# Kernel tuning notes

Measured on AMD Instinct MI355X. Metric: run time of the kernel, lower is better.

The kernel has to match this reference:

```python
import jax, jax.numpy as jnp
import numpy as np

T, B, E, H = 2048, 2, 1024, 16
D = E // H
MAX_REL = 16  # RelativePosition default max_relative_position


def setup_inputs() -> dict:
    key = jax.random.key(0)
    ks = jax.random.split(key, 11)
    s = 1.0 / np.sqrt(E)
    inp = {
        'query': jax.random.normal(ks[0], (T, B, E), dtype=jnp.float32),
        'Wq': jax.random.normal(ks[1], (E, E), dtype=jnp.float32) * s,
        'bq': jnp.zeros((E,), dtype=jnp.float32),
        'Wk': jax.random.normal(ks[2], (E, E), dtype=jnp.float32) * s,
        'bk': jnp.zeros((E,), dtype=jnp.float32),
        'Wv': jax.random.normal(ks[3], (E, E), dtype=jnp.float32) * s,
        'bv': jnp.zeros((E,), dtype=jnp.float32),
        'Wo': jax.random.normal(ks[4], (E, E), dtype=jnp.float32) * s,
        'bo': jnp.zeros((E,), dtype=jnp.float32),
        'rk_table': jax.random.normal(ks[5], (2 * MAX_REL + 1, D), dtype=jnp.float32) * 0.05,
        'rv_table': jax.random.normal(ks[6], (2 * MAX_REL + 1, D), dtype=jnp.float32) * 0.05,
    }
    return inp


def _rel_idx(lq, lk):
    # distance_mat = k - q, clipped to [-MAX_REL, MAX_REL], shifted to [0, 2*MAX_REL]
    d = jnp.arange(lk)[None, :] - jnp.arange(lq)[:, None]
    return jnp.clip(d, -MAX_REL, MAX_REL) + MAX_REL  # [lq, lk] int


def reference(query, Wq, bq, Wk, bk, Wv, bv, Wo, bo, rk_table, rv_table):
    t, b, e = query.shape
    scale = D ** -0.5
    # projections (torch Linear: x @ W.T + b)
    q = (query @ Wq.T + bq) * scale
    k = query @ Wk.T + bk
    v = query @ Wv.T + bv
    # [T,B,E] -> [B*H, T, D]
    q = q.reshape(t, b * H, D).transpose(1, 0, 2)
    k = k.reshape(t, b * H, D).transpose(1, 0, 2)
    v = v.reshape(t, b * H, D).transpose(1, 0, 2)
    # content scores + Shaw relative-position key scores
    scores = jnp.einsum('ntd,nsd->nts', q, k)            # [N, T, S]
    rk = rk_table[_rel_idx(t, t)]                        # [T, S, D]
    scores = scores + jnp.einsum('ntd,tsd->nts', q, rk)  # relpos_k term
    probs = jax.nn.softmax(scores, axis=-1)
    # weighted values + Shaw relative-position value term
    rv = rv_table[_rel_idx(t, t)]                        # [T, S, D]
    attn = jnp.einsum('nts,nsd->ntd', probs, v) + jnp.einsum('nts,tsd->ntd', probs, rv)
    # [B*H, T, D] -> [T, B, E]
    attn = attn.transpose(1, 0, 2).reshape(t, b, e)
    return attn @ Wo.T + bo
```

## Files before the change

kernel.cpp:

```cpp
#include <hip/hip_runtime.h>
#include <hip/hip_bf16.h>
#include <math.h>

#define T_   2048
#define B_   2
#define E_   1024
#define H_   16
#define D_   64
#define NH_  32
#define M_   4096

typedef __attribute__((ext_vector_type(8))) short s8b;
typedef __attribute__((ext_vector_type(4))) float f4;

#define MFMA_B16(a,b,c) __builtin_amdgcn_mfma_f32_16x16x32_bf16(a,b,c,0,0,0)
#define LOG2E 1.44269504088896f

__device__ __forceinline__ unsigned short f2bu(float f) {
    union { __hip_bfloat16 h; unsigned short u; } cv;
    cv.h = __float2bfloat16(f);
    return cv.u;
}
__device__ __forceinline__ float bu2f(unsigned short u) {
    union { __hip_bfloat16 h; unsigned short u; } cv; cv.u = u;
    return __bfloat162float(cv.h);
}
__device__ __forceinline__ unsigned int pk2(float a, float b) {
    return (unsigned int)f2bu(a) | ((unsigned int)f2bu(b) << 16);
}
__device__ __forceinline__ float ld1d(const void* p, size_t idx, bool f32) {
    return f32 ? ((const float*)p)[idx] : bu2f(((const unsigned short*)p)[idx]);
}
__device__ __forceinline__ float qsum16(float v) {
    v += __shfl_xor(v, 1); v += __shfl_xor(v, 2);
    v += __shfl_xor(v, 4); v += __shfl_xor(v, 8);
    return v;
}

__global__ void detect_dtype(const unsigned short* __restrict__ q, int* __restrict__ flag) {
    int e = (q[threadIdx.x] >> 7) & 0xFF;
    bool sane = (e == 0) || (e >= 97 && e <= 157);
    unsigned long long m = __ballot(sane);
    if (threadIdx.x == 0) *flag = (__popcll(m) >= 56) ? 0 : 1;
}

__global__ __launch_bounds__(256) void cvt_bf16(
    const void* __restrict__ x,
    const void* __restrict__ Wq, const void* __restrict__ Wk,
    const void* __restrict__ Wv, const void* __restrict__ Wo,
    const void* __restrict__ bq, const void* __restrict__ bk,
    const void* __restrict__ bv, const void* __restrict__ bo,
    unsigned short* __restrict__ xw, unsigned short* __restrict__ Ww,
    unsigned short* __restrict__ bw, const int* __restrict__ flag)
{
    const bool f32m = (*flag != 0);
    const int y = blockIdx.y;
    const void* src; unsigned short* dst; int n;
    if (y == 0)      { src = x; dst = xw; n = M_ * E_; }
    else if (y <= 4) {
        src = (y == 1) ? Wq : (y == 2) ? Wk : (y == 3) ? Wv : Wo;
        dst = Ww + (size_t)(y - 1) * E_ * E_; n = E_ * E_;
    } else {
        src = (y == 5) ? bq : (y == 6) ? bk : (y == 7) ? bv : bo;
        dst = bw + (size_t)(y - 5) * E_; n = E_;
    }
    int i = (blockIdx.x * 256 + threadIdx.x) * 8;
    if (i >= n) return;
    if (f32m) {
        const float* s = (const float*)src + i;
        float4 f0 = *(const float4*)s, f1 = *(const float4*)(s + 4);
        union { unsigned int d[4]; s8b v; } u;
        u.d[0] = pk2(f0.x, f0.y); u.d[1] = pk2(f0.z, f0.w);
        u.d[2] = pk2(f1.x, f1.y); u.d[3] = pk2(f1.z, f1.w);
        *(s8b*)(dst + i) = u.v;
    } else {
        *(s8b*)(dst + i) = *(const s8b*)((const unsigned short*)src + i);
    }
}

__global__ __launch_bounds__(256, 3) void qkv_gemm(
    const unsigned short* __restrict__ xw, const unsigned short* __restrict__ Ww,
    const unsigned short* __restrict__ bw,
    unsigned short* __restrict__ qo, unsigned short* __restrict__ ko,
    unsigned short* __restrict__ vo)
{
    const int bid = blockIdx.x;
    const int r = bid & 7, s = bid >> 3;
    const int g = r + 8 * (s >> 3);
    const int e0 = (s & 7) * 128;
    const int m0 = (g & 31) * 128;
    const int p  = g >> 5;
    const unsigned short* W    = Ww + (size_t)p * E_ * E_;
    const unsigned short* bias = bw + (size_t)p * E_;
    unsigned short* dst = (p == 0) ? qo : (p == 1) ? ko : vo;
    const float scale = (p == 0) ? 0.125f * LOG2E : 1.0f;

    const int tid = threadIdx.x, w = tid >> 6, lane = tid & 63;
    const int quad = lane >> 4, lc = lane & 15;
    const int wx = w & 1, wy = w >> 1;

    __shared__ unsigned short a_s[2][128 * 36];
    __shared__ unsigned short b_s[2][128 * 36];

    f4 acc[4][4];
    #pragma unroll
    for (int i = 0; i < 4; i++)
        #pragma unroll
        for (int j = 0; j < 4; j++) acc[i][j] = (f4){0.f, 0.f, 0.f, 0.f};

    const int lrow = tid >> 1, lcb = (tid & 1) * 16;
    const size_t abase = (size_t)(m0 + lrow) * E_ + lcb;
    const size_t bbase = (size_t)(e0 + lrow) * E_ + lcb;

    s8b pA0 = *(const s8b*)(xw + abase);
    s8b pA1 = *(const s8b*)(xw + abase + 8);
    s8b pB0 = *(const s8b*)(W + bbase);
    s8b pB1 = *(const s8b*)(W + bbase + 8);
    *(s8b*)&a_s[0][lrow * 36 + lcb]     = pA0;
    *(s8b*)&a_s[0][lrow * 36 + lcb + 8] = pA1;
    *(s8b*)&b_s[0][lrow * 36 + lcb]     = pB0;
    *(s8b*)&b_s[0][lrow * 36 + lcb + 8] = pB1;
    __syncthreads();

    for (int k0 = 0; k0 < E_; k0 += 32) {
        const int cur = (k0 >> 5) & 1;
        if (k0 + 32 < E_) {
            pA0 = *(const s8b*)(xw + abase + k0 + 32);
            pA1 = *(const s8b*)(xw + abase + k0 + 40);
            pB0 = *(const s8b*)(W + bbase + k0 + 32);
            pB1 = *(const s8b*)(W + bbase + k0 + 40);
        }
        s8b af[4], bfr[4];
        #pragma unroll
        for (int i = 0; i < 4; i++) af[i]  = *(const s8b*)&a_s[cur][(wy*64 + i*16 + lc)*36 + quad*8];
        #pragma unroll
        for (int i = 0; i < 4; i++) bfr[i] = *(const s8b*)&b_s[cur][(wx*64 + i*16 + lc)*36 + quad*8];
        #pragma unroll
        for (int ms = 0; ms < 4; ms++)
            #pragma unroll
            for (int ns = 0; ns < 4; ns++)
                acc[ms][ns] = MFMA_B16(af[ms], bfr[ns], acc[ms][ns]);
        if (k0 + 32 < E_) {
            *(s8b*)&a_s[cur ^ 1][lrow * 36 + lcb]     = pA0;
            *(s8b*)&a_s[cur ^ 1][lrow * 36 + lcb + 8] = pA1;
            *(s8b*)&b_s[cur ^ 1][lrow * 36 + lcb]     = pB0;
            *(s8b*)&b_s[cur ^ 1][lrow * 36 + lcb + 8] = pB1;
        }
        __syncthreads();
    }

    float bias_v[4];
    #pragma unroll
    for (int ns = 0; ns < 4; ns++) bias_v[ns] = bu2f(bias[e0 + wx*64 + ns*16 + lc]);

    #pragma unroll
    for (int ms = 0; ms < 4; ms++)
        #pragma unroll
        for (int ns = 0; ns < 4; ns++)
            #pragma unroll
            for (int r2 = 0; r2 < 4; r2++) {
                float val = (acc[ms][ns][r2] + bias_v[ns]) * scale;
                float nb = __shfl_xor(val, 1);
                if (!(lane & 1)) {
                    int m = m0 + wy*64 + ms*16 + quad*4 + r2;
                    int t = m >> 1, bb = m & 1;
                    int e = e0 + wx*64 + ns*16 + lc;
                    int h = e >> 6, d = e & 63;
                    *(unsigned int*)&dst[(((size_t)(bb*H_ + h) * T_ + t) << 6) + d] = pk2(val, nb);
                }
            }
}

__global__ __launch_bounds__(256, 2) void attn_mfma(
    const unsigned short* __restrict__ q, const unsigned short* __restrict__ k,
    const unsigned short* __restrict__ v,
    const void* __restrict__ rk_t, const void* __restrict__ rv_t,
    unsigned short* __restrict__ aout, const int* __restrict__ flag)
{
    const bool f32m = (*flag != 0);
    const int bid = blockIdx.x;
    const int n = bid & 31, qt = bid >> 5;
    const int t0 = qt * 128;
    const int tid = threadIdx.x, w = tid >> 6, lane = tid & 63;
    const int quad = lane >> 4, lc = lane & 15;

    __shared__ unsigned short k_s[2][64 * 72];
    __shared__ unsigned short v_t[2][64 * 72];
    __shared__ unsigned short p_s[4][32 * 72];
    __shared__ unsigned short qrk_s[128 * 36];
    __shared__ unsigned short diag16[128 * 33];
    __shared__ float st_L[128], st_R[128];

    const unsigned short* qn = q + ((size_t)n * T_ + t0) * D_;
    const unsigned short* kn = k + (size_t)n * T_ * D_;
    const unsigned short* vn = v + (size_t)n * T_ * D_;

    s8b qa[2][2];
    #pragma unroll
    for (int mt = 0; mt < 2; mt++)
        #pragma unroll
        for (int kf = 0; kf < 2; kf++)
            qa[mt][kf] = *(const s8b*)(qn + (size_t)(w*32 + mt*16 + lc) * D_ + kf*32 + quad*8);

    for (int i = tid; i < 128 * 33; i += 256) diag16[i] = 0;

    unsigned int* rks = (unsigned int*)&p_s[0][0];
    for (int i = tid; i < 48 * 36; i += 256) {
        int r = i / 36, c2 = i % 36;
        unsigned int val = 0;
        if (r < 33 && c2 < 32)
            val = pk2(ld1d(rk_t, r*64 + 2*c2, f32m), ld1d(rk_t, r*64 + 2*c2 + 1, f32m));
        rks[i] = val;
    }
    __syncthreads();

    #pragma unroll
    for (int mt = 0; mt < 2; mt++)
        for (int nt = 0; nt < 3; nt++) {
            s8b b0 = *(const s8b*)((const unsigned short*)rks + (nt*16 + lc)*72 + quad*8);
            s8b b1 = *(const s8b*)((const unsigned short*)rks + (nt*16 + lc)*72 + 32 + quad*8);
            f4 a = (f4){0.f, 0.f, 0.f, 0.f};
            a = MFMA_B16(qa[mt][0], b0, a);
            a = MFMA_B16(qa[mt][1], b1, a);
            #pragma unroll
            for (int r = 0; r < 4; r++) {
                float nb = __shfl_xor(a[r], 1);
                int col = nt*16 + lc;
                if (!(lane & 1) && col < 34)
                    ((unsigned int*)qrk_s)[(w*32 + mt*16 + quad*4 + r)*18 + (col >> 1)] = pk2(a[r], nb);
            }
        }
    __syncthreads();

    float qL[2][4], qR[2][4];
    float L_p[2][4] = {}, R_p[2][4] = {};
    f4 O[2][4], lsN[2], lsL[2], lsR[2];
    #pragma unroll
    for (int mt = 0; mt < 2; mt++) {
        #pragma unroll
        for (int r = 0; r < 4; r++) {
            int row = w*32 + mt*16 + quad*4 + r;
            qL[mt][r] = bu2f(qrk_s[row*36 + 0]);
            qR[mt][r] = bu2f(qrk_s[row*36 + 32]);
        }
        lsN[mt] = (f4){0.f, 0.f, 0.f, 0.f};
        lsL[mt] = (f4){0.f, 0.f, 0.f, 0.f};
        lsR[mt] = (f4){0.f, 0.f, 0.f, 0.f};
        #pragma unroll
        for (int dt = 0; dt < 4; dt++) O[mt][dt] = (f4){0.f, 0.f, 0.f, 0.f};
    }
    const short ob = (short)0x3F80;
    const s8b ones = { ob, ob, ob, ob, ob, ob, ob, ob };

    const int ks_ = tid >> 2, kdq = (tid & 3) * 16;
    const int vsp = (tid & 31) * 2, vd0 = (tid >> 5) * 8;
    s8b kr0 = *(const s8b*)(kn + ks_*64 + kdq);
    s8b kr1 = *(const s8b*)(kn + ks_*64 + kdq + 8);
    s8b vr0 = *(const s8b*)(vn + vsp*64 + vd0);
    s8b vr1 = *(const s8b*)(vn + (vsp + 1)*64 + vd0);
    *(s8b*)&k_s[0][ks_*72 + kdq]     = kr0;
    *(s8b*)&k_s[0][ks_*72 + kdq + 8] = kr1;
    #pragma unroll
    for (int i = 0; i < 8; i++)
        ((unsigned int*)v_t[0])[(vd0 + i)*36 + (vsp >> 1)] =
            (unsigned int)(unsigned short)vr0[i] | ((unsigned int)(unsigned short)vr1[i] << 16);
    __syncthreads();

    for (int kt = 0; kt < 32; kt++) {
        const int s0 = kt * 64;
        const int cur = kt & 1;
        if (kt + 1 < 32) {
            const unsigned short* kp = kn + (size_t)(s0 + 64) * D_;
            const unsigned short* vp = vn + (size_t)(s0 + 64) * D_;
            kr0 = *(const s8b*)(kp + ks_*64 + kdq);
            kr1 = *(const s8b*)(kp + ks_*64 + kdq + 8);
            vr0 = *(const s8b*)(vp + vsp*64 + vd0);
            vr1 = *(const s8b*)(vp + (vsp + 1)*64 + vd0);
        }

        const bool farL  = (s0 + 63 < t0 - 16);
        const bool farR  = (s0 > t0 + 143);
        const bool nearT = !farL && !farR;

        s8b bk[4][2];
        #pragma unroll
        for (int st = 0; st < 4; st++) {
            bk[st][0] = *(const s8b*)&k_s[cur][(st*16 + lc)*72 + quad*8];
            bk[st][1] = *(const s8b*)&k_s[cur][(st*16 + lc)*72 + 32 + quad*8];
        }

        #pragma unroll
        for (int mt = 0; mt < 2; mt++) {
            if (!nearT) {
                const float* qb = farL ? qL[mt] : qR[mt];
                f4 ini = (f4){qb[0], qb[1], qb[2], qb[3]};
                #pragma unroll
                for (int st = 0; st < 4; st++) {
                    f4 a = MFMA_B16(qa[mt][0], bk[st][0], ini);
                    a = MFMA_B16(qa[mt][1], bk[st][1], a);
                    #pragma unroll
                    for (int r = 0; r < 4; r++)
                        p_s[w][(mt*16 + quad*4 + r)*72 + st*16 + lc] = f2bu(exp2f(a[r]));
                }
            } else {
                #pragma unroll
                for (int st = 0; st < 4; st++) {
                    f4 a = (f4){0.f, 0.f, 0.f, 0.f};
                    a = MFMA_B16(qa[mt][0], bk[st][0], a);
                    a = MFMA_B16(qa[mt][1], bk[st][1], a);
                    #pragma unroll
                    for (int r = 0; r < 4; r++) {
                        int t_l = w*32 + mt*16 + quad*4 + r;
                        int rel = (s0 + st*16 + lc) - (t0 + t_l);
                        int rc = rel < -16 ? -16 : (rel > 16 ? 16 : rel);
                        float e = exp2f(a[r] + bu2f(qrk_s[t_l*36 + rc + 16]));
                        unsigned short eb = f2bu(e);
                        if (rel <= -16)      L_p[mt][r] += e;
                        else if (rel >= 16)  R_p[mt][r] += e;
                        else                 diag16[t_l*33 + rel + 15] = eb;
                        p_s[w][(mt*16 + quad*4 + r)*72 + st*16 + lc] = eb;
                    }
                }
            }
        }

        s8b pa[2][2];
        #pragma unroll
        for (int mt = 0; mt < 2; mt++) {
            pa[mt][0] = *(const s8b*)&p_s[w][(mt*16 + lc)*72 + quad*8];
            pa[mt][1] = *(const s8b*)&p_s[w][(mt*16 + lc)*72 + 32 + quad*8];
        }
        if (nearT) {
            #pragma unroll
            for (int mt = 0; mt < 2; mt++) {
                lsN[mt] = MFMA_B16(pa[mt][0], ones, lsN[mt]);
                lsN[mt] = MFMA_B16(pa[mt][1], ones, lsN[mt]);
            }
        } else if (farL) {
            #pragma unroll
            for (int mt = 0; mt < 2; mt++) {
                lsL[mt] = MFMA_B16(pa[mt][0], ones, lsL[mt]);
                lsL[mt] = MFMA_B16(pa[mt][1], ones, lsL[mt]);
            }
        } else {
            #pragma unroll
            for (int mt = 0; mt < 2; mt++) {
                lsR[mt] = MFMA_B16(pa[mt][0], ones, lsR[mt]);
                lsR[mt] = MFMA_B16(pa[mt][1], ones, lsR[mt]);
            }
        }
        #pragma unroll
        for (int dt = 0; dt < 4; dt++) {
            s8b b0 = *(const s8b*)&v_t[cur][(dt*16 + lc)*72 + quad*8];
            s8b b1 = *(const s8b*)&v_t[cur][(dt*16 + lc)*72 + 32 + quad*8];
            O[0][dt] = MFMA_B16(pa[0][0], b0, O[0][dt]);
            O[0][dt] = MFMA_B16(pa[0][1], b1, O[0][dt]);
            O[1][dt] = MFMA_B16(pa[1][0], b0, O[1][dt]);
            O[1][dt] = MFMA_B16(pa[1][1], b1, O[1][dt]);
        }

        if (kt + 1 < 32) {
            *(s8b*)&k_s[cur ^ 1][ks_*72 + kdq]     = kr0;
            *(s8b*)&k_s[cur ^ 1][ks_*72 + kdq + 8] = kr1;
            #pragma unroll
            for (int i = 0; i < 8; i++)
                ((unsigned int*)v_t[cur ^ 1])[(vd0 + i)*36 + (vsp >> 1)] =
                    (unsigned int)(unsigned short)vr0[i] | ((unsigned int)(unsigned short)vr1[i] << 16);
        }
        __syncthreads();
    }

    float linv[2][4];
    #pragma unroll
    for (int mt = 0; mt < 2; mt++)
        #pragma unroll
        for (int r = 0; r < 4; r++) {
            float l = lsN[mt][r] + lsL[mt][r] + lsR[mt][r];
            float L = lsL[mt][r] + qsum16(L_p[mt][r]);
            float R = lsR[mt][r] + qsum16(R_p[mt][r]);
            linv[mt][r] = 1.f / l;
            if (lc == 0) {
                int row = w*32 + mt*16 + quad*4 + r;
                st_L[row] = L; st_R[row] = R;
            }
        }
    {
        unsigned int* rvs = (unsigned int*)&k_s[0][0];
        for (int i = tid; i < 64 * 36; i += 256) {
            int d = i / 36, c2 = i % 36;
            int r0 = 2 * c2, r1 = 2 * c2 + 1;
            float x0 = (r0 < 33) ? ld1d(rv_t, (size_t)r0 * 64 + d, f32m) : 0.f;
            float x1 = (r1 < 33) ? ld1d(rv_t, (size_t)r1 * 64 + d, f32m) : 0.f;
            rvs[i] = pk2(x0, x1);
        }
    }
    __syncthreads();
    for (int j = 0; j < 32; j++) {
        int c = lane;
        int row = w*32 + j;
        unsigned short pv;
        if (c == 0)        pv = f2bu(st_L[row]);
        else if (c == 32)  pv = f2bu(st_R[row]);
        else if (c < 32)   pv = diag16[row*33 + c - 1];
        else               pv = 0;
        p_s[w][j*72 + c] = pv;
    }
    s8b pa[2][2];
    #pragma unroll
    for (int mt = 0; mt < 2; mt++) {
        pa[mt][0] = *(const s8b*)&p_s[w][(mt*16 + lc)*72 + quad*8];
        pa[mt][1] = *(const s8b*)&p_s[w][(mt*16 + lc)*72 + 32 + quad*8];
    }
    #pragma unroll
    for (int dt = 0; dt < 4; dt++) {
        s8b b0 = *(const s8b*)&k_s[0][(dt*16 + lc)*72 + quad*8];
        s8b b1 = *(const s8b*)&k_s[0][(dt*16 + lc)*72 + 32 + quad*8];
        O[0][dt] = MFMA_B16(pa[0][0], b0, O[0][dt]);
        O[0][dt] = MFMA_B16(pa[0][1], b1, O[0][dt]);
        O[1][dt] = MFMA_B16(pa[1][0], b0, O[1][dt]);
        O[1][dt] = MFMA_B16(pa[1][1], b1, O[1][dt]);
    }
    const int bb = n >> 4, h = n & 15;
    #pragma unroll
    for (int mt = 0; mt < 2; mt++)
        #pragma unroll
        for (int r = 0; r < 4; r++) {
            int t_g = t0 + w*32 + mt*16 + quad*4 + r;
            #pragma unroll
            for (int dt = 0; dt < 4; dt++) {
                float val = O[mt][dt][r] * linv[mt][r];
                float nb = __shfl_xor(val, 1);
                if (!(lane & 1)) {
                    int e = h*64 + dt*16 + lc;
                    *(unsigned int*)&aout[((size_t)t_g * B_ + bb) * E_ + e] = pk2(val, nb);
                }
            }
        }
}

__global__ __launch_bounds__(256, 3) void out_gemm(
    const unsigned short* __restrict__ A,
    const unsigned short* __restrict__ Wob, const unsigned short* __restrict__ bob,
    void* __restrict__ out, const int* __restrict__ flag)
{
    const bool f32m = (*flag != 0);
    const int bid = blockIdx.x;
    const int r = bid & 7, s = bid >> 3;
    const int g = r + 8 * (s >> 3);
    const int m0 = g * 128;
    const int e0 = (s & 7) * 128;

    const int tid = threadIdx.x, w = tid >> 6, lane = tid & 63;
    const int quad = lane >> 4, lc = lane & 15;
    const int wx = w & 1, wy = w >> 1;

    __shared__ unsigned short a_s[2][128 * 36];
    __shared__ unsigned short b_s[2][128 * 36];

    f4 acc[4][4];
    #pragma unroll
    for (int i = 0; i < 4; i++)
        #pragma unroll
        for (int j = 0; j < 4; j++) acc[i][j] = (f4){0.f, 0.f, 0.f, 0.f};

    const int lrow = tid >> 1, lcb = (tid & 1) * 16;
    const size_t abase = (size_t)(m0 + lrow) * E_ + lcb;
    const size_t bbase = (size_t)(e0 + lrow) * E_ + lcb;

    s8b pA0 = *(const s8b*)(A + abase);
    s8b pA1 = *(const s8b*)(A + abase + 8);
    s8b pB0 = *(const s8b*)(Wob + bbase);
    s8b pB1 = *(const s8b*)(Wob + bbase + 8);
    *(s8b*)&a_s[0][lrow*36 + lcb]     = pA0;
    *(s8b*)&a_s[0][lrow*36 + lcb + 8] = pA1;
    *(s8b*)&b_s[0][lrow*36 + lcb]     = pB0;
    *(s8b*)&b_s[0][lrow*36 + lcb + 8] = pB1;
    __syncthreads();

    for (int k0 = 0; k0 < E_; k0 += 32) {
        const int cur = (k0 >> 5) & 1;
        if (k0 + 32 < E_) {
            pA0 = *(const s8b*)(A + abase + k0 + 32);
            pA1 = *(const s8b*)(A + abase + k0 + 40);
            pB0 = *(const s8b*)(Wob + bbase + k0 + 32);
            pB1 = *(const s8b*)(Wob + bbase + k0 + 40);
        }
        s8b af[4], bfr[4];
        #pragma unroll
        for (int i = 0; i < 4; i++) af[i]  = *(const s8b*)&a_s[cur][(wy*64 + i*16 + lc)*36 + quad*8];
        #pragma unroll
        for (int i = 0; i < 4; i++) bfr[i] = *(const s8b*)&b_s[cur][(wx*64 + i*16 + lc)*36 + quad*8];
        #pragma unroll
        for (int ms = 0; ms < 4; ms++)
            #pragma unroll
            for (int ns = 0; ns < 4; ns++)
                acc[ms][ns] = MFMA_B16(af[ms], bfr[ns], acc[ms][ns]);
        if (k0 + 32 < E_) {
            *(s8b*)&a_s[cur ^ 1][lrow*36 + lcb]     = pA0;
            *(s8b*)&a_s[cur ^ 1][lrow*36 + lcb + 8] = pA1;
            *(s8b*)&b_s[cur ^ 1][lrow*36 + lcb]     = pB0;
            *(s8b*)&b_s[cur ^ 1][lrow*36 + lcb + 8] = pB1;
        }
        __syncthreads();
    }

    float bias_v[4];
    #pragma unroll
    for (int ns = 0; ns < 4; ns++) bias_v[ns] = bu2f(bob[e0 + wx*64 + ns*16 + lc]);

    #pragma unroll
    for (int ms = 0; ms < 4; ms++)
        #pragma unroll
        for (int ns = 0; ns < 4; ns++)
            #pragma unroll
            for (int r2 = 0; r2 < 4; r2++) {
                float val = acc[ms][ns][r2] + bias_v[ns];
                size_t m = m0 + wy*64 + ms*16 + quad*4 + r2;
                int e = e0 + wx*64 + ns*16 + lc;
                if (f32m) {
                    ((float*)out)[m * E_ + e] = val;
                } else {
                    float nb = __shfl_xor(val, 1);
                    if (!(lane & 1))
                        *(unsigned int*)&((unsigned short*)out)[m * E_ + e] = pk2(val, nb);
                }
            }
}

extern "C" void kernel_launch(void* const* d_in, const int* in_sizes, int n_in,
                              void* d_out, int out_size, void* d_ws, size_t ws_size,
                              hipStream_t stream) {
    const void* x  = d_in[0];
    const void* Wq = d_in[1];  const void* bq = d_in[2];
    const void* Wk = d_in[3];  const void* bk = d_in[4];
    const void* Wv = d_in[5];  const void* bv = d_in[6];
    const void* Wo = d_in[7];  const void* bo = d_in[8];
    const void* rk = d_in[9];  const void* rv = d_in[10];

    int* flag = (int*)d_ws;
    const size_t HTD = (size_t)NH_ * T_ * D_;
    unsigned short* qw = (unsigned short*)((char*)d_ws + 256);
    unsigned short* kw = qw + HTD;
    unsigned short* vw = kw + HTD;
    unsigned short* aw = vw + HTD;
    unsigned short* xw = aw + (size_t)M_ * E_;
    unsigned short* Ww = xw + (size_t)M_ * E_;
    unsigned short* bw = Ww + (size_t)4 * E_ * E_;

    detect_dtype<<<1, 64, 0, stream>>>((const unsigned short*)x, flag);
    cvt_bf16<<<dim3((M_*E_/8 + 255)/256, 9), 256, 0, stream>>>(
        x, Wq, Wk, Wv, Wo, bq, bk, bv, bo, xw, Ww, bw, flag);
    qkv_gemm<<<dim3(768), 256, 0, stream>>>(xw, Ww, bw, qw, kw, vw);
    attn_mfma<<<dim3(NH_ * (T_/128)), 256, 0, stream>>>(qw, kw, vw, rk, rv, aw, flag);
    out_gemm<<<dim3(256), 256, 0, stream>>>(aw, Ww + (size_t)3*E_*E_, bw + 3*E_,
                                            d_out, flag);
}
```

Before: 256.3 us.

## Use direct global-to-LDS loads with XOR swizzle and pre-transpose V in QKV GEMM

Replaces register-staged global loads followed by LDS stores with global_load_lds direct transfers in the QKV GEMM, the attention K/V tiles and the output GEMM. Padded LDS rows give way to an XOR swizzle so MFMA fragment reads avoid bank conflicts. The QKV epilogue now writes V in a [n,d,t] transposed layout, so the attention kernel no longer transposes V in shared memory. The exp-probability conversion to bf16 also switches to a fast bias-add truncation in place of the library conversion. This removes register pressure and LDS write instructions, but it depends on the asynchronous-load semantics being correctly fenced by the existing barriers.

```diff
diff --git a/kernel.cpp b/kernel.cpp
--- a/kernel.cpp
+++ b/kernel.cpp
@@ -21,6 +21,9 @@
     cv.h = __float2bfloat16(f);
     return cv.u;
 }
+__device__ __forceinline__ unsigned short f2bu_fast(float f) {
+    return (unsigned short)((__float_as_uint(f) + 0x8000u) >> 16);
+}
 __device__ __forceinline__ float bu2f(unsigned short u) {
     union { __hip_bfloat16 h; unsigned short u; } cv; cv.u = u;
     return __bfloat162float(cv.h);
@@ -35,6 +38,11 @@
     v += __shfl_xor(v, 1); v += __shfl_xor(v, 2);
     v += __shfl_xor(v, 4); v += __shfl_xor(v, 8);
     return v;
+}
+__device__ __forceinline__ void glds16(const unsigned short* g, unsigned short* l) {
+    __builtin_amdgcn_global_load_lds(
+        (const __attribute__((address_space(1))) unsigned int*)g,
+        (__attribute__((address_space(3))) unsigned int*)l, 16, 0, 0);
 }
 
 __global__ void detect_dtype(const unsigned short* __restrict__ q, int* __restrict__ flag) {
@@ -85,22 +93,21 @@
     unsigned short* __restrict__ vo)
 {
     const int bid = blockIdx.x;
-    const int r = bid & 7, s = bid >> 3;
-    const int g = r + 8 * (s >> 3);
-    const int e0 = (s & 7) * 128;
+    const int r_ = bid & 7, s_ = bid >> 3;
+    const int g = r_ + 8 * (s_ >> 3);
+    const int e0 = (s_ & 7) * 128;
     const int m0 = (g & 31) * 128;
     const int p  = g >> 5;
     const unsigned short* W    = Ww + (size_t)p * E_ * E_;
     const unsigned short* bias = bw + (size_t)p * E_;
-    unsigned short* dst = (p == 0) ? qo : (p == 1) ? ko : vo;
     const float scale = (p == 0) ? 0.125f * LOG2E : 1.0f;
 
     const int tid = threadIdx.x, w = tid >> 6, lane = tid & 63;
     const int quad = lane >> 4, lc = lane & 15;
     const int wx = w & 1, wy = w >> 1;
 
-    __shared__ unsigned short a_s[2][128 * 36];
-    __shared__ unsigned short b_s[2][128 * 36];
+    __shared__ unsigned short a_s[2][128 * 32];
+    __shared__ unsigned short b_s[2][128 * 32];
 
     f4 acc[4][4];
     #pragma unroll
@@ -108,44 +115,40 @@
         #pragma unroll
         for (int j = 0; j < 4; j++) acc[i][j] = (f4){0.f, 0.f, 0.f, 0.f};
 
-    const int lrow = tid >> 1, lcb = (tid & 1) * 16;
-    const size_t abase = (size_t)(m0 + lrow) * E_ + lcb;
-    const size_t bbase = (size_t)(e0 + lrow) * E_ + lcb;
-
-    s8b pA0 = *(const s8b*)(xw + abase);
-    s8b pA1 = *(const s8b*)(xw + abase + 8);
-    s8b pB0 = *(const s8b*)(W + bbase);
-    s8b pB1 = *(const s8b*)(W + bbase + 8);
-    *(s8b*)&a_s[0][lrow * 36 + lcb]     = pA0;
-    *(s8b*)&a_s[0][lrow * 36 + lcb + 8] = pA1;
-    *(s8b*)&b_s[0][lrow * 36 + lcb]     = pB0;
-    *(s8b*)&b_s[0][lrow * 36 + lcb + 8] = pB1;
+    const int gr = lane >> 2;
+    const int gc = (lane & 3) ^ ((lane >> 2) & 3);
+    const size_t aoff = (size_t)(m0 + w*32 + gr) * E_ + gc*8;
+    const size_t boff = (size_t)(e0 + w*32 + gr) * E_ + gc*8;
+
+    #pragma unroll
+    for (int j = 0; j < 2; j++) {
+        glds16(xw + aoff + (size_t)j*16*E_, &a_s[0][(w*128 + j*64) * 8]);
+        glds16(W  + boff + (size_t)j*16*E_, &b_s[0][(w*128 + j*64) * 8]);
+    }
     __syncthreads();
 
+    const int fcA = quad ^ (lc & 3);
     for (int k0 = 0; k0 < E_; k0 += 32) {
         const int cur = (k0 >> 5) & 1;
         if (k0 + 32 < E_) {
-            pA0 = *(const s8b*)(xw + abase + k0 + 32);
-            pA1 = *(const s8b*)(xw + abase + k0 + 40);
-            pB0 = *(const s8b*)(W + bbase + k0 + 32);
-            pB1 = *(const s8b*)(W + bbase + k0 + 40);
+            #pragma unroll
+            for (int j = 0; j < 2; j++) {
+                glds16(xw + aoff + (size_t)j*16*E_ + k0 + 32, &a_s[cur^1][(w*128 + j*64) * 8]);
+                glds16(W  + boff + (size_t)j*16*E_ + k0 + 32, &b_s[cur^1][(w*128 + j*64) * 8]);
+            }
         }
         s8b af[4], bfr[4];
         #pragma unroll
-        for (int i = 0; i < 4; i++) af[i]  = *(const s8b*)&a_s[cur][(wy*64 + i*16 + lc)*36 + quad*8];
-        #pragma unroll
-        for (int i = 0; i < 4; i++) bfr[i] = *(const s8b*)&b_s[cur][(wx*64 + i*16 + lc)*36 + quad*8];
+        for (int i = 0; i < 4; i++)
+            af[i]  = *(const s8b*)&a_s[cur][((wy*64 + i*16 + lc)*4 + fcA) * 8];
+        #pragma unroll
+        for (int i = 0; i < 4; i++)
+            bfr[i] = *(const s8b*)&b_s[cur][((wx*64 + i*16 + lc)*4 + fcA) * 8];
         #pragma unroll
         for (int ms = 0; ms < 4; ms++)
             #pragma unroll
             for (int ns = 0; ns < 4; ns++)
                 acc[ms][ns] = MFMA_B16(af[ms], bfr[ns], acc[ms][ns]);
-        if (k0 + 32 < E_) {
-            *(s8b*)&a_s[cur ^ 1][lrow * 36 + lcb]     = pA0;
-            *(s8b*)&a_s[cur ^ 1][lrow * 36 + lcb + 8] = pA1;
-            *(s8b*)&b_s[cur ^ 1][lrow * 36 + lcb]     = pB0;
-            *(s8b*)&b_s[cur ^ 1][lrow * 36 + lcb + 8] = pB1;
-        }
         __syncthreads();
     }
 
@@ -153,22 +156,41 @@
     #pragma unroll
     for (int ns = 0; ns < 4; ns++) bias_v[ns] = bu2f(bias[e0 + wx*64 + ns*16 + lc]);
 
-    #pragma unroll
-    for (int ms = 0; ms < 4; ms++)
-        #pragma unroll
-        for (int ns = 0; ns < 4; ns++)
-            #pragma unroll
-            for (int r2 = 0; r2 < 4; r2++) {
-                float val = (acc[ms][ns][r2] + bias_v[ns]) * scale;
-                float nb = __shfl_xor(val, 1);
-                if (!(lane & 1)) {
-                    int m = m0 + wy*64 + ms*16 + quad*4 + r2;
-                    int t = m >> 1, bb = m & 1;
-                    int e = e0 + wx*64 + ns*16 + lc;
-                    int h = e >> 6, d = e & 63;
-                    *(unsigned int*)&dst[(((size_t)(bb*H_ + h) * T_ + t) << 6) + d] = pk2(val, nb);
+    if (p < 2) {
+        #pragma unroll
+        for (int ms = 0; ms < 4; ms++)
+            #pragma unroll
+            for (int ns = 0; ns < 4; ns++)
+                #pragma unroll
+                for (int r2 = 0; r2 < 4; r2++) {
+                    float val = (acc[ms][ns][r2] + bias_v[ns]) * scale;
+                    float nb = __shfl_xor(val, 1);
+                    if (!(lane & 1)) {
+                        int m = m0 + wy*64 + ms*16 + quad*4 + r2;
+                        int t = m >> 1, bb = m & 1;
+                        int e = e0 + wx*64 + ns*16 + lc;
+                        int h = e >> 6, d = e & 63;
+                        unsigned short* dst = (p == 0) ? qo : ko;
+                        *(unsigned int*)&dst[(((size_t)(bb*H_ + h) * T_ + t) << 6) + d] = pk2(val, nb);
+                    }
                 }
-            }
+    } else {
+        #pragma unroll
+        for (int ms = 0; ms < 4; ms++) {
+            int t0v = (m0 + wy*64 + ms*16 + quad*4) >> 1;
+            #pragma unroll
+            for (int ns = 0; ns < 4; ns++) {
+                int e = e0 + wx*64 + ns*16 + lc;
+                int h = e >> 6, d = e & 63;
+                float v0 = acc[ms][ns][0] + bias_v[ns];
+                float v1 = acc[ms][ns][1] + bias_v[ns];
+                float v2 = acc[ms][ns][2] + bias_v[ns];
+                float v3 = acc[ms][ns][3] + bias_v[ns];
+                *(unsigned int*)&vo[((size_t)h        * 64 + d) * T_ + t0v] = pk2(v0, v2);
+                *(unsigned int*)&vo[((size_t)(H_ + h) * 64 + d) * T_ + t0v] = pk2(v1, v3);
+            }
+        }
+    }
 }
 
 __global__ __launch_bounds__(256, 2) void attn_mfma(
@@ -184,8 +206,8 @@
     const int tid = threadIdx.x, w = tid >> 6, lane = tid & 63;
     const int quad = lane >> 4, lc = lane & 15;
 
-    __shared__ unsigned short k_s[2][64 * 72];
-    __shared__ unsigned short v_t[2][64 * 72];
+    __shared__ unsigned short k_s[2][64 * 64];
+    __shared__ unsigned short v_s[2][64 * 64];
     __shared__ unsigned short p_s[4][32 * 72];
     __shared__ unsigned short qrk_s[128 * 36];
     __shared__ unsigned short diag16[128 * 33];
@@ -193,7 +215,7 @@
 
     const unsigned short* qn = q + ((size_t)n * T_ + t0) * D_;
     const unsigned short* kn = k + (size_t)n * T_ * D_;
-    const unsigned short* vn = v + (size_t)n * T_ * D_;
+    const unsigned short* vn = v + (size_t)n * D_ * T_;
 
     s8b qa[2][2];
     #pragma unroll
@@ -252,30 +274,28 @@
     const short ob = (short)0x3F80;
     const s8b ones = { ob, ob, ob, ob, ob, ob, ob, ob };
 
-    const int ks_ = tid >> 2, kdq = (tid & 3) * 16;
-    const int vsp = (tid & 31) * 2, vd0 = (tid >> 5) * 8;
-    s8b kr0 = *(const s8b*)(kn + ks_*64 + kdq);
-    s8b kr1 = *(const s8b*)(kn + ks_*64 + kdq + 8);
-    s8b vr0 = *(const s8b*)(vn + vsp*64 + vd0);
-    s8b vr1 = *(const s8b*)(vn + (vsp + 1)*64 + vd0);
-    *(s8b*)&k_s[0][ks_*72 + kdq]     = kr0;
-    *(s8b*)&k_s[0][ks_*72 + kdq + 8] = kr1;
-    #pragma unroll
-    for (int i = 0; i < 8; i++)
-        ((unsigned int*)v_t[0])[(vd0 + i)*36 + (vsp >> 1)] =
-            (unsigned int)(unsigned short)vr0[i] | ((unsigned int)(unsigned short)vr1[i] << 16);
+    const int grr = lane >> 3;
+    const int gcc = (lane & 7) ^ (lane >> 3);
+    const size_t koff = (size_t)(w*16 + grr) * D_ + gcc*8;
+    const size_t voff = (size_t)(w*16 + grr) * T_ + gcc*8;
+
+    #pragma unroll
+    for (int j = 0; j < 2; j++) {
+        glds16(kn + koff + (size_t)j*8*D_, &k_s[0][(w*128 + j*64) * 8]);
+        glds16(vn + voff + (size_t)j*8*T_, &v_s[0][(w*128 + j*64) * 8]);
+    }
     __syncthreads();
 
+    const int lc7 = lc & 7;
     for (int kt = 0; kt < 32; kt++) {
         const int s0 = kt * 64;
         const int cur = kt & 1;
         if (kt + 1 < 32) {
-            const unsigned short* kp = kn + (size_t)(s0 + 64) * D_;
-            const unsigned short* vp = vn + (size_t)(s0 + 64) * D_;
-            kr0 = *(const s8b*)(kp + ks_*64 + kdq);
-            kr1 = *(const s8b*)(kp + ks_*64 + kdq + 8);
-            vr0 = *(const s8b*)(vp + vsp*64 + vd0);
-            vr1 = *(const s8b*)(vp + (vsp + 1)*64 + vd0);
+            #pragma unroll
+            for (int j = 0; j < 2; j++) {
+                glds16(kn + koff + (size_t)(s0 + 64 + j*8)*D_, &k_s[cur^1][(w*128 + j*64) * 8]);
+                glds16(vn + voff + (size_t)j*8*T_ + s0 + 64,  &v_s[cur^1][(w*128 + j*64) * 8]);
+            }
         }
 
         const bool farL  = (s0 + 63 < t0 - 16);
@@ -285,8 +305,9 @@
         s8b bk[4][2];
         #pragma unroll
         for (int st = 0; st < 4; st++) {
-            bk[st][0] = *(const s8b*)&k_s[cur][(st*16 + lc)*72 + quad*8];
-            bk[st][1] = *(const s8b*)&k_s[cur][(st*16 + lc)*72 + 32 + quad*8];
+            int row = st*16 + lc;
+            bk[st][0] = *(const s8b*)&k_s[cur][(row*8 + (quad       ^ lc7)) * 8];
+            bk[st][1] = *(const s8b*)&k_s[cur][(row*8 + ((4 + quad) ^ lc7)) * 8];
         }
 
         #pragma unroll
@@ -300,7 +321,7 @@
                     a = MFMA_B16(qa[mt][1], bk[st][1], a);
                     #pragma unroll
                     for (int r = 0; r < 4; r++)
-                        p_s[w][(mt*16 + quad*4 + r)*72 + st*16 + lc] = f2bu(exp2f(a[r]));
+                        p_s[w][(mt*16 + quad*4 + r)*72 + st*16 + lc] = f2bu_fast(exp2f(a[r]));
                 }
             } else {
                 #pragma unroll
@@ -314,7 +335,7 @@
                         int rel = (s0 + st*16 + lc) - (t0 + t_l);
                         int rc = rel < -16 ? -16 : (rel > 16 ? 16 : rel);
                         float e = exp2f(a[r] + bu2f(qrk_s[t_l*36 + rc + 16]));
-                        unsigned short eb = f2bu(e);
+                        unsigned short eb = f2bu_fast(e);
                         if (rel <= -16)      L_p[mt][r] += e;
                         else if (rel >= 16)  R_p[mt][r] += e;
                         else                 diag16[t_l*33 + rel + 15] = eb;
@@ -351,21 +372,13 @@
         }
         #pragma unroll
         for (int dt = 0; dt < 4; dt++) {
-            s8b b0 = *(const s8b*)&v_t[cur][(dt*16 + lc)*72 + quad*8];
-            s8b b1 = *(const s8b*)&v_t[cur][(dt*16 + lc)*72 + 32 + quad*8];
+            int row = dt*16 + lc;
+            s8b b0 = *(const s8b*)&v_s[cur][(row*8 + (quad       ^ lc7)) * 8];
+            s8b b1 = *(const s8b*)&v_s[cur][(row*8 + ((4 + quad) ^ lc7)) * 8];
             O[0][dt] = MFMA_B16(pa[0][0], b0, O[0][dt]);
             O[0][dt] = MFMA_B16(pa[0][1], b1, O[0][dt]);
             O[1][dt] = MFMA_B16(pa[1][0], b0, O[1][dt]);
             O[1][dt] = MFMA_B16(pa[1][1], b1, O[1][dt]);
-        }
-
-        if (kt + 1 < 32) {
-            *(s8b*)&k_s[cur ^ 1][ks_*72 + kdq]     = kr0;
-            *(s8b*)&k_s[cur ^ 1][ks_*72 + kdq + 8] = kr1;
-            #pragma unroll
-            for (int i = 0; i < 8; i++)
-                ((unsigned int*)v_t[cur ^ 1])[(vd0 + i)*36 + (vsp >> 1)] =
-                    (unsigned int)(unsigned short)vr0[i] | ((unsigned int)(unsigned short)vr1[i] << 16);
         }
         __syncthreads();
     }
@@ -386,12 +399,13 @@
         }
     {
         unsigned int* rvs = (unsigned int*)&k_s[0][0];
-        for (int i = tid; i < 64 * 36; i += 256) {
-            int d = i / 36, c2 = i % 36;
-            int r0 = 2 * c2, r1 = 2 * c2 + 1;
+        for (int i = tid; i < 64 * 32; i += 256) {
+            int d = i >> 5, dwL = i & 31;
+            int r0 = dwL * 2, r1 = r0 + 1;
             float x0 = (r0 < 33) ? ld1d(rv_t, (size_t)r0 * 64 + d, f32m) : 0.f;
             float x1 = (r1 < 33) ? ld1d(rv_t, (size_t)r1 * 64 + d, f32m) : 0.f;
-            rvs[i] = pk2(x0, x1);
+            int phys = d * 32 + ((dwL >> 2) ^ (d & 7)) * 4 + (dwL & 3);
+            rvs[phys] = pk2(x0, x1);
         }
     }
     __syncthreads();
@@ -413,8 +427,9 @@
     }
     #pragma unroll
     for (int dt = 0; dt < 4; dt++) {
-        s8b b0 = *(const s8b*)&k_s[0][(dt*16 + lc)*72 + quad*8];
-        s8b b1 = *(const s8b*)&k_s[0][(dt*16 + lc)*72 + 32 + quad*8];
+        int row = dt*16 + lc;
+        s8b b0 = *(const s8b*)&k_s[0][(row*8 + (quad       ^ lc7)) * 8];
+        s8b b1 = *(const s8b*)&k_s[0][(row*8 + ((4 + quad) ^ lc7)) * 8];
         O[0][dt] = MFMA_B16(pa[0][0], b0, O[0][dt]);
         O[0][dt] = MFMA_B16(pa[0][1], b1, O[0][dt]);
         O[1][dt] = MFMA_B16(pa[1][0], b0, O[1][dt]);
@@ -445,17 +460,17 @@
 {
     const bool f32m = (*flag != 0);
     const int bid = blockIdx.x;
-    const int r = bid & 7, s = bid >> 3;
-    const int g = r + 8 * (s >> 3);
+    const int r_ = bid & 7, s_ = bid >> 3;
+    const int g = r_ + 8 * (s_ >> 3);
     const int m0 = g * 128;
-    const int e0 = (s & 7) * 128;
+    const int e0 = (s_ & 7) * 128;
 
     const int tid = threadIdx.x, w = tid >> 6, lane = tid & 63;
     const int quad = lane >> 4, lc = lane & 15;
     const int wx = w & 1, wy = w >> 1;
 
-    __shared__ unsigned short a_s[2][128 * 36];
-    __shared__ unsigned short b_s[2][128 * 36];
+    __shared__ unsigned short a_s[2][128 * 32];
+    __shared__ unsigned short b_s[2][128 * 32];
 
     f4 acc[4][4];
     #pragma unroll
@@ -463,44 +478,40 @@
         #pragma unroll
         for (int j = 0; j < 4; j++) acc[i][j] = (f4){0.f, 0.f, 0.f, 0.f};
 
-    const int lrow = tid >> 1, lcb = (tid & 1) * 16;
-    const size_t abase = (size_t)(m0 + lrow) * E_ + lcb;
-    const size_t bbase = (size_t)(e0 + lrow) * E_ + lcb;
-
-    s8b pA0 = *(const s8b*)(A + abase);
-    s8b pA1 = *(const s8b*)(A + abase + 8);
-    s8b pB0 = *(const s8b*)(Wob + bbase);
-    s8b pB1 = *(const s8b*)(Wob + bbase + 8);
-    *(s8b*)&a_s[0][lrow*36 + lcb]     = pA0;
-    *(s8b*)&a_s[0][lrow*36 + lcb + 8] = pA1;
-    *(s8b*)&b_s[0][lrow*36 + lcb]     = pB0;
-    *(s8b*)&b_s[0][lrow*36 + lcb + 8] = pB1;
+    const int gr = lane >> 2;
+    const int gc = (lane & 3) ^ ((lane >> 2) & 3);
+    const size_t aoff = (size_t)(m0 + w*32 + gr) * E_ + gc*8;
+    const size_t boff = (size_t)(e0 + w*32 + gr) * E_ + gc*8;
+
+    #pragma unroll
+    for (int j = 0; j < 2; j++) {
+        glds16(A   + aoff + (size_t)j*16*E_, &a_s[0][(w*128 + j*64) * 8]);
+        glds16(Wob + boff + (size_t)j*16*E_, &b_s[0][(w*128 + j*64) * 8]);
+    }
     __syncthreads();
 
+    const int fcA = quad ^ (lc & 3);
     for (int k0 = 0; k0 < E_; k0 += 32) {
         const int cur = (k0 >> 5) & 1;
         if (k0 + 32 < E_) {
-            pA0 = *(const s8b*)(A + abase + k0 + 32);
-            pA1 = *(const s8b*)(A + abase + k0 + 40);
-            pB0 = *(const s8b*)(Wob + bbase + k0 + 32);
-            pB1 = *(const s8b*)(Wob + bbase + k0 + 40);
+            #pragma unroll
+            for (int j = 0; j < 2; j++) {
+                glds16(A   + aoff + (size_t)j*16*E_ + k0 + 32, &a_s[cur^1][(w*128 + j*64) * 8]);
+                glds16(Wob + boff + (size_t)j*16*E_ + k0 + 32, &b_s[cur^1][(w*128 + j*64) * 8]);
+            }
         }
         s8b af[4], bfr[4];
         #pragma unroll
-        for (int i = 0; i < 4; i++) af[i]  = *(const s8b*)&a_s[cur][(wy*64 + i*16 + lc)*36 + quad*8];
-        #pragma unroll
-        for (int i = 0; i < 4; i++) bfr[i] = *(const s8b*)&b_s[cur][(wx*64 + i*16 + lc)*36 + quad*8];
+        for (int i = 0; i < 4; i++)
+            af[i]  = *(const s8b*)&a_s[cur][((wy*64 + i*16 + lc)*4 + fcA) * 8];
+        #pragma unroll
+        for (int i = 0; i < 4; i++)
+            bfr[i] = *(const s8b*)&b_s[cur][((wx*64 + i*16 + lc)*4 + fcA) * 8];
         #pragma unroll
         for (int ms = 0; ms < 4; ms++)
             #pragma unroll
             for (int ns = 0; ns < 4; ns++)
                 acc[ms][ns] = MFMA_B16(af[ms], bfr[ns], acc[ms][ns]);
-        if (k0 + 32 < E_) {
-            *(s8b*)&a_s[cur ^ 1][lrow*36 + lcb]     = pA0;
-            *(s8b*)&a_s[cur ^ 1][lrow*36 + lcb + 8] = pA1;
-            *(s8b*)&b_s[cur ^ 1][lrow*36 + lcb]     = pB0;
-            *(s8b*)&b_s[cur ^ 1][lrow*36 + lcb + 8] = pB1;
-        }
         __syncthreads();
     }
 
```

After: 256.2 us. No clear change (-0.1%).
